# Performance work log

Hardware: AMD Instinct MI355X
Metric: run time of the kernel (lower is better)

The kernel has to match this reference:

```python
import jax, jax.numpy as jnp
import numpy as np

NUM_GROUPS = 32
NUM_HEADS = 8
EPS = 1e-5


def setup_inputs() -> dict:
    key = jax.random.key(0)
    ks = jax.random.split(key, 4)
    b, c, h, w = 16, 512, 32, 32
    x = jax.random.normal(ks[0], (b, c, h, w), dtype=jnp.float32)
    norm_w = jnp.ones((c,), dtype=jnp.float32)
    norm_b = jnp.zeros((c,), dtype=jnp.float32)
    qkv_w = jax.random.normal(ks[1], (3 * c, c), dtype=jnp.float32) * (1.0 / np.sqrt(c))
    qkv_b = jnp.zeros((3 * c,), dtype=jnp.float32)
    proj_w = jax.random.normal(ks[2], (c, c), dtype=jnp.float32) * (1.0 / np.sqrt(c))
    proj_b = jnp.zeros((c,), dtype=jnp.float32)
    return {"x": x, "norm_w": norm_w, "norm_b": norm_b,
            "qkv_w": qkv_w, "qkv_b": qkv_b, "proj_w": proj_w, "proj_b": proj_b}


def group_norm(x, weight, bias):
    b, c, h, w = x.shape
    xg = x.reshape(b, NUM_GROUPS, c // NUM_GROUPS, h * w)
    mean = xg.mean(axis=(2, 3), keepdims=True)
    var = xg.var(axis=(2, 3), keepdims=True)
    xn = (xg - mean) * jax.lax.rsqrt(var + EPS)
    xn = xn.reshape(b, c, h, w)
    return xn * weight[None, :, None, None] + bias[None, :, None, None]


def reference(x, norm_w, norm_b, qkv_w, qkv_b, proj_w, proj_b):
    b, c, h, w = x.shape
    n = h * w
    head = NUM_HEADS
    ch = c // head

    x_norm = group_norm(x, norm_w, norm_b)
    # 1x1 conv == channel matmul: [b,3c,n]
    xf = x_norm.reshape(b, c, n)
    qkv = jnp.einsum('oc,bcn->bon', qkv_w, xf) + qkv_b[None, :, None]
    q, k, v = jnp.split(qkv, 3, axis=1)  # each [b,c,n]
    q = q.reshape(b, head, ch, n) * (ch ** -0.5)
    k = k.reshape(b, head, ch, n)
    v = v.reshape(b, head, ch, n)

    attn = jnp.einsum('bhcn,bhcm->bhnm', q, k)
    attn = jax.nn.softmax(attn, axis=-1)
    out = jnp.einsum('bhnm,bhcm->bhcn', attn, v)  # [b,head,ch,n]
    out = out.reshape(b, c, n)
    out = jnp.einsum('oc,bcn->bon', proj_w, out) + proj_b[None, :, None]
    return x + out.reshape(b, c, h, w)
```

## Files before the change

### kernel.cpp

```cpp
#include <hip/hip_runtime.h>

typedef short short8 __attribute__((ext_vector_type(8)));
typedef float f32x4 __attribute__((ext_vector_type(4)));

#define B_   16
#define C_   512
#define N_   1024
#define NH_  8
#define CH_  64
#define G_   32
#define CPG_ 16

__device__ inline float b2f(unsigned int u) {
    union { unsigned int i; float f; } v; v.i = u << 16; return v.f;
}
__device__ inline unsigned short f2b(float f) {
    union { float f; unsigned int i; } v; v.f = f;
    unsigned int r = v.i + 0x7fffu + ((v.i >> 16) & 1u);
    return (unsigned short)(r >> 16);
}
__device__ inline unsigned int pack2(float a, float b) {
    return (unsigned int)f2b(a) | ((unsigned int)f2b(b) << 16);
}
__device__ inline unsigned int asu(float f) {
    union { float f; unsigned int i; } v; v.f = f; return v.i;
}
__device__ inline unsigned int packtr(float a, float b) {
    return __builtin_amdgcn_perm(asu(b), asu(a), 0x07060302u);
}

__global__ __launch_bounds__(256) void conv_w(const float* __restrict__ qkvw,
                                              const float* __restrict__ projw,
                                              unsigned short* __restrict__ wq,
                                              unsigned short* __restrict__ wp)
{
    const int NQ = 3 * C_ * C_;
    int idx = (blockIdx.x * 256 + threadIdx.x) * 8;
    const float* src; unsigned short* dst; int j;
    if (idx < NQ) { src = qkvw; dst = wq; j = idx; }
    else          { src = projw; dst = wp; j = idx - NQ; }
    float4 u0 = *(const float4*)(src + j);
    float4 u1 = *(const float4*)(src + j + 4);
    uint4 p;
    p.x = pack2(u0.x, u0.y); p.y = pack2(u0.z, u0.w);
    p.z = pack2(u1.x, u1.y); p.w = pack2(u1.z, u1.w);
    *(uint4*)(dst + j) = p;
}

__global__ __launch_bounds__(256) void gn_kernel(const float* __restrict__ x,
                                                 const float* __restrict__ nw,
                                                 const float* __restrict__ nb,
                                                 unsigned short* __restrict__ xnT)
{
    int b = blockIdx.x >> 5, g = blockIdx.x & 31;
    int t = threadIdx.x;
    const float* base = x + ((size_t)(b * C_ + g * CPG_)) * N_;

    float s = 0.f, ss = 0.f;
    for (int it = 0; it < 16; ++it) {
        int idx = (it * 256 + t) * 4;
        float4 u = *(const float4*)(base + idx);
        s  += u.x + u.y + u.z + u.w;
        ss += u.x * u.x + u.y * u.y + u.z * u.z + u.w * u.w;
    }
#pragma unroll
    for (int off = 1; off < 64; off <<= 1) {
        s  += __shfl_xor(s, off);
        ss += __shfl_xor(ss, off);
    }
    __shared__ float red[8];
    int wv = t >> 6;
    if ((t & 63) == 0) { red[wv * 2] = s; red[wv * 2 + 1] = ss; }
    __syncthreads();
    s  = red[0] + red[2] + red[4] + red[6];
    ss = red[1] + red[3] + red[5] + red[7];
    float mean = s * (1.f / 16384.f);
    float var  = ss * (1.f / 16384.f) - mean * mean;
    float rstd = rsqrtf(var + 1e-5f);

    int cl = t >> 4, nn4 = (t & 15) * 4;
    float sc = nw[g * CPG_ + cl] * rstd;
    float sh = nb[g * CPG_ + cl] - mean * sc;
    int nlB = t >> 2, c4 = (t & 3) * 4;

    __shared__ unsigned short T[64 * 17];
    for (int ch = 0; ch < 16; ++ch) {
        int n0 = ch * 64;
        float4 u = *(const float4*)(base + (size_t)cl * N_ + n0 + nn4);
        T[(nn4 + 0) * 17 + cl] = f2b(u.x * sc + sh);
        T[(nn4 + 1) * 17 + cl] = f2b(u.y * sc + sh);
        T[(nn4 + 2) * 17 + cl] = f2b(u.z * sc + sh);
        T[(nn4 + 3) * 17 + cl] = f2b(u.w * sc + sh);
        __syncthreads();
        ushort4 o;
        o.x = T[nlB * 17 + c4 + 0];
        o.y = T[nlB * 17 + c4 + 1];
        o.z = T[nlB * 17 + c4 + 2];
        o.w = T[nlB * 17 + c4 + 3];
        *(ushort4*)(xnT + ((size_t)(b * N_ + n0 + nlB)) * C_ + g * CPG_ + c4) = o;
        __syncthreads();
    }
}

__global__ __launch_bounds__(256) void qkv_kernel(const unsigned short* __restrict__ w,
                                                  const float* __restrict__ bias,
                                                  const unsigned short* __restrict__ xnT,
                                                  unsigned short* __restrict__ qT,
                                                  unsigned short* __restrict__ kT,
                                                  unsigned short* __restrict__ vv)
{
    const int LDA = 40;
    __shared__ unsigned short Als[128 * 40], Bls[128 * 40];
    int t = threadIdx.x;
    int n0 = blockIdx.x * 128, m0 = blockIdx.y * 128, b = blockIdx.z;
    int lane = t & 63, wv = t >> 6;
    int l = lane & 15, qd = lane >> 4;
    int wm = (wv >> 1) * 64, wn = (wv & 1) * 64;
    f32x4 acc[4][4] = {};
    const unsigned short* Bbase = xnT + ((size_t)(b * N_ + n0)) * C_;

    for (int kk = 0; kk < 16; ++kk) {
#pragma unroll
        for (int s_ = 0; s_ < 2; ++s_) {
            int idx = s_ * 256 + t;
            int row = idx >> 2, c8 = (idx & 3) * 8;
            *(uint4*)&Als[row * LDA + c8] = *(const uint4*)(w + (size_t)(m0 + row) * C_ + kk * 32 + c8);
            *(uint4*)&Bls[row * LDA + c8] = *(const uint4*)(Bbase + (size_t)row * C_ + kk * 32 + c8);
        }
        __syncthreads();
        short8 aF[4], bF[4];
#pragma unroll
        for (int i = 0; i < 4; ++i) {
            aF[i] = *(const short8*)&Als[(wm + i * 16 + l) * LDA + qd * 8];
            bF[i] = *(const short8*)&Bls[(wn + i * 16 + l) * LDA + qd * 8];
        }
#pragma unroll
        for (int mt = 0; mt < 4; ++mt)
#pragma unroll
            for (int nt = 0; nt < 4; ++nt)
                acc[mt][nt] = __builtin_amdgcn_mfma_f32_16x16x32_bf16(aF[mt], bF[nt], acc[mt][nt], 0, 0, 0);
        __syncthreads();
    }

    int o_base = m0 + wm;
    int sec = o_base >> 9;
    int oc = o_base & 511;
    int h = oc >> 6;
    float bv[4][4];
#pragma unroll
    for (int mt = 0; mt < 4; ++mt)
#pragma unroll
        for (int r = 0; r < 4; ++r)
            bv[mt][r] = bias[o_base + mt * 16 + qd * 4 + r];

    if (sec < 2) {
        unsigned short* dst = (sec == 0) ? qT : kT;
        float scl = (sec == 0) ? (0.125f * 1.44269504f) : 1.0f;
#pragma unroll
        for (int mt = 0; mt < 4; ++mt)
#pragma unroll
            for (int nt = 0; nt < 4; ++nt) {
                int n = n0 + wn + nt * 16 + l;
                ushort4 o;
                o.x = f2b((acc[mt][nt][0] + bv[mt][0]) * scl);
                o.y = f2b((acc[mt][nt][1] + bv[mt][1]) * scl);
                o.z = f2b((acc[mt][nt][2] + bv[mt][2]) * scl);
                o.w = f2b((acc[mt][nt][3] + bv[mt][3]) * scl);
                *(ushort4*)(dst + ((size_t)(b * NH_ + h) * N_ + n) * CH_ + mt * 16 + qd * 4) = o;
            }
    } else {
#pragma unroll
        for (int mt = 0; mt < 4; ++mt)
#pragma unroll
            for (int nt = 0; nt < 4; ++nt) {
                int n = n0 + wn + nt * 16 + l;
#pragma unroll
                for (int r = 0; r < 4; ++r) {
                    int ch = mt * 16 + qd * 4 + r;
                    vv[((size_t)(b * NH_ + h) * CH_ + ch) * N_ + n] = f2b(acc[mt][nt][r] + bv[mt][r]);
                }
            }
    }
}

__global__ __launch_bounds__(256, 4) void attn_kernel(const unsigned short* __restrict__ qT,
                                                      const unsigned short* __restrict__ kT,
                                                      const unsigned short* __restrict__ vv,
                                                      unsigned short* __restrict__ at)
{
    __shared__ unsigned short Ks[2][4096];
    __shared__ unsigned short Vs[2][4096];

    int t = threadIdx.x, lane = t & 63, wv = t >> 6;
    int l = lane & 15, qd = lane >> 4;
    int blk = blockIdx.x;
    int ibk = blk >> 7;
    int bh  = blk & 127;
    int h = bh & 7, b = bh >> 3;
    int i0 = ibk * 128 + wv * 32;
    const size_t hoff = (size_t)bh * (size_t)N_ * CH_;
    const unsigned short* qbase = qT + hoff;
    const unsigned short* kbase = kT + hoff;
    const unsigned short* vbase = vv + hoff;

    short8 qF[2][2];
#pragma unroll
    for (int it = 0; it < 2; ++it)
#pragma unroll
        for (int ks = 0; ks < 2; ++ks)
            qF[it][ks] = *(const short8*)(qbase + (size_t)(i0 + it * 16 + l) * CH_ + ks * 32 + qd * 8);

    int srow = t >> 2, sc16 = (t & 3) * 16;
    int sw = srow & 7, bb = (t & 3) * 2;
    int d0 = srow * 64 + ((bb ^ sw) * 8);
    int d1 = srow * 64 + (((bb + 1) ^ sw) * 8);
    const unsigned short* kSrc = kbase + (size_t)srow * CH_ + sc16;
    const unsigned short* vSrc = vbase + (size_t)srow * N_ + sc16;

    f32x4 Oa[4][2] = {};
    float lsum[2] = {0.f, 0.f};
    int la0 = (qd & 1) * 32 + l;
    int la1 = la0 + 16;
    int swl = l & 7;

    uint4 ku0, ku1, vu0, vu1;
    {
        const uint4* kp = (const uint4*)(kSrc);
        ku0 = kp[0]; ku1 = kp[1];
        const uint4* vp2 = (const uint4*)(vSrc);
        vu0 = vp2[0]; vu1 = vp2[1];
        *(uint4*)&Ks[0][d0] = ku0; *(uint4*)&Ks[0][d1] = ku1;
        *(uint4*)&Vs[0][d0] = vu0; *(uint4*)&Vs[0][d1] = vu1;
        kp  = (const uint4*)(kSrc + 4096);
        ku0 = kp[0]; ku1 = kp[1];
        vp2 = (const uint4*)(vSrc + 64);
        vu0 = vp2[0]; vu1 = vp2[1];
    }

    for (int tile = 0; tile < 16; ++tile) {
        __syncthreads();
        if (tile < 15) {
            unsigned short* Kw = Ks[(tile + 1) & 1];
            unsigned short* Vw = Vs[(tile + 1) & 1];
            *(uint4*)&Kw[d0] = ku0; *(uint4*)&Kw[d1] = ku1;
            *(uint4*)&Vw[d0] = vu0; *(uint4*)&Vw[d1] = vu1;
            if (tile < 14) {
                const uint4* kp = (const uint4*)(kSrc + (size_t)(tile + 2) * 4096);
                ku0 = kp[0]; ku1 = kp[1];
                const uint4* vp2 = (const uint4*)(vSrc + (size_t)(tile + 2) * 64);
                vu0 = vp2[0]; vu1 = vp2[1];
            }
        }
        const unsigned short* Kb = Ks[tile & 1];
        const unsigned short* Vb = Vs[tile & 1];
#pragma unroll
        for (int jb = 0; jb < 2; ++jb) {
            short8 kA[2][2];
#pragma unroll
            for (int jt = 0; jt < 2; ++jt)
#pragma unroll
                for (int ks = 0; ks < 2; ++ks)
                    kA[jt][ks] = *(const short8*)&Kb[(jb * 32 + jt * 16 + l) * 64 + (((ks * 4 + qd) ^ swl) * 8)];
            f32x4 Sa[2][2] = {};
#pragma unroll
            for (int jt = 0; jt < 2; ++jt)
#pragma unroll
                for (int it = 0; it < 2; ++it)
#pragma unroll
                    for (int ks = 0; ks < 2; ++ks)
                        Sa[jt][it] = __builtin_amdgcn_mfma_f32_16x16x32_bf16(kA[jt][ks], qF[it][ks], Sa[jt][it], 0, 0, 0);
            unsigned int pk[2][2][2];
#pragma unroll
            for (int jt = 0; jt < 2; ++jt)
#pragma unroll
                for (int it = 0; it < 2; ++it) {
                    float p0 = __builtin_amdgcn_exp2f(Sa[jt][it][0]);
                    float p1 = __builtin_amdgcn_exp2f(Sa[jt][it][1]);
                    float p2 = __builtin_amdgcn_exp2f(Sa[jt][it][2]);
                    float p3 = __builtin_amdgcn_exp2f(Sa[jt][it][3]);
                    lsum[it] += (p0 + p1) + (p2 + p3);
                    pk[jt][it][0] = packtr(p0, p1);
                    pk[jt][it][1] = packtr(p2, p3);
                }
            short8 bP[2];
#pragma unroll
            for (int it = 0; it < 2; ++it) {
                union { short8 s; unsigned int u[4]; } fb;
                unsigned int a0 = (unsigned int)__shfl((int)pk[0][it][0], la0);
                unsigned int b0 = (unsigned int)__shfl((int)pk[1][it][0], la0);
                fb.u[0] = (qd < 2) ? a0 : b0;
                unsigned int a1 = (unsigned int)__shfl((int)pk[0][it][1], la0);
                unsigned int b1 = (unsigned int)__shfl((int)pk[1][it][1], la0);
                fb.u[1] = (qd < 2) ? a1 : b1;
                unsigned int a2 = (unsigned int)__shfl((int)pk[0][it][0], la1);
                unsigned int b2 = (unsigned int)__shfl((int)pk[1][it][0], la1);
                fb.u[2] = (qd < 2) ? a2 : b2;
                unsigned int a3 = (unsigned int)__shfl((int)pk[0][it][1], la1);
                unsigned int b3 = (unsigned int)__shfl((int)pk[1][it][1], la1);
                fb.u[3] = (qd < 2) ? a3 : b3;
                bP[it] = fb.s;
            }
            short8 vA[4];
#pragma unroll
            for (int cht = 0; cht < 4; ++cht)
                vA[cht] = *(const short8*)&Vb[(cht * 16 + l) * 64 + (((jb * 4 + qd) ^ swl) * 8)];
#pragma unroll
            for (int cht = 0; cht < 4; ++cht)
#pragma unroll
                for (int it = 0; it < 2; ++it)
                    Oa[cht][it] = __builtin_amdgcn_mfma_f32_16x16x32_bf16(vA[cht], bP[it], Oa[cht][it], 0, 0, 0);
        }
    }

#pragma unroll
    for (int it = 0; it < 2; ++it) {
        float lt = lsum[it];
        lt += __shfl_xor(lt, 16);
        lt += __shfl_xor(lt, 32);
        float inv = 1.0f / lt;
        int i = i0 + it * 16 + l;
        unsigned short* dst = at + ((size_t)(b * N_ + i)) * C_ + h * CH_;
#pragma unroll
        for (int cht = 0; cht < 4; ++cht) {
            ushort4 o;
            o.x = f2b(Oa[cht][it][0] * inv);
            o.y = f2b(Oa[cht][it][1] * inv);
            o.z = f2b(Oa[cht][it][2] * inv);
            o.w = f2b(Oa[cht][it][3] * inv);
            *(ushort4*)(dst + cht * 16 + qd * 4) = o;
        }
    }
}

__global__ __launch_bounds__(256) void proj_kernel(const unsigned short* __restrict__ w,
                                                   const float* __restrict__ bias,
                                                   const unsigned short* __restrict__ at,
                                                   const float* __restrict__ x,
                                                   float* __restrict__ out)
{
    const int LDA = 40;
    __shared__ unsigned short Als[128 * 40], Bls[128 * 40];
    int t = threadIdx.x;
    int n0 = blockIdx.x * 128, m0 = blockIdx.y * 128, b = blockIdx.z;
    int lane = t & 63, wv = t >> 6;
    int l = lane & 15, qd = lane >> 4;
    int wm = (wv >> 1) * 64, wn = (wv & 1) * 64;
    f32x4 acc[4][4] = {};
    const unsigned short* Bbase = at + ((size_t)(b * N_ + n0)) * C_;

    for (int kk = 0; kk < 16; ++kk) {
#pragma unroll
        for (int s_ = 0; s_ < 2; ++s_) {
            int idx = s_ * 256 + t;
            int row = idx >> 2, c8 = (idx & 3) * 8;
            *(uint4*)&Als[row * LDA + c8] = *(const uint4*)(w + (size_t)(m0 + row) * C_ + kk * 32 + c8);
            *(uint4*)&Bls[row * LDA + c8] = *(const uint4*)(Bbase + (size_t)row * C_ + kk * 32 + c8);
        }
        __syncthreads();
        short8 aF[4], bF[4];
#pragma unroll
        for (int i = 0; i < 4; ++i) {
            aF[i] = *(const short8*)&Als[(wm + i * 16 + l) * LDA + qd * 8];
            bF[i] = *(const short8*)&Bls[(wn + i * 16 + l) * LDA + qd * 8];
        }
#pragma unroll
        for (int mt = 0; mt < 4; ++mt)
#pragma unroll
            for (int nt = 0; nt < 4; ++nt)
                acc[mt][nt] = __builtin_amdgcn_mfma_f32_16x16x32_bf16(aF[mt], bF[nt], acc[mt][nt], 0, 0, 0);
        __syncthreads();
    }

    float bv[4][4];
#pragma unroll
    for (int mt = 0; mt < 4; ++mt)
#pragma unroll
        for (int r = 0; r < 4; ++r)
            bv[mt][r] = bias[m0 + wm + mt * 16 + qd * 4 + r];

#pragma unroll
    for (int mt = 0; mt < 4; ++mt)
#pragma unroll
        for (int nt = 0; nt < 4; ++nt) {
            int n = n0 + wn + nt * 16 + l;
#pragma unroll
            for (int r = 0; r < 4; ++r) {
                int o = m0 + wm + mt * 16 + qd * 4 + r;
                size_t idx = ((size_t)b * C_ + o) * N_ + n;
                out[idx] = acc[mt][nt][r] + bv[mt][r] + x[idx];
            }
        }
}

extern "C" void kernel_launch(void* const* d_in, const int* in_sizes, int n_in,
                              void* d_out, int out_size, void* d_ws, size_t ws_size,
                              hipStream_t stream) {
    const float* x     = (const float*)d_in[0];
    const float* nw    = (const float*)d_in[1];
    const float* nb    = (const float*)d_in[2];
    const float* qkvw  = (const float*)d_in[3];
    const float* qkvb  = (const float*)d_in[4];
    const float* projw = (const float*)d_in[5];
    const float* projb = (const float*)d_in[6];
    float* out = (float*)d_out;
    char* ws = (char*)d_ws;
    const size_t SZ = (size_t)B_ * N_ * C_ * 2;
    unsigned short* xnT = (unsigned short*)(ws);
    unsigned short* qTp = (unsigned short*)(ws + SZ);
    unsigned short* kTp = (unsigned short*)(ws + 2 * SZ);
    unsigned short* vp  = (unsigned short*)(ws + 3 * SZ);
    unsigned short* atp = (unsigned short*)(ws);
    unsigned short* wq  = (unsigned short*)(ws + 4 * SZ);
    unsigned short* wp  = (unsigned short*)(ws + 4 * SZ + (size_t)3 * C_ * C_ * 2);

    hipLaunchKernelGGL(conv_w,      dim3(512), dim3(256), 0, stream, qkvw, projw, wq, wp);
    hipLaunchKernelGGL(gn_kernel,   dim3(B_ * G_), dim3(256), 0, stream, x, nw, nb, xnT);
    hipLaunchKernelGGL(qkv_kernel,  dim3(8, 12, B_), dim3(256), 0, stream, wq, qkvb, xnT, qTp, kTp, vp);
    hipLaunchKernelGGL(attn_kernel, dim3(1024), dim3(256), 0, stream, qTp, kTp, vp, atp);
    hipLaunchKernelGGL(proj_kernel, dim3(8, 4, B_), dim3(256), 0, stream, wp, projb, atp, x, out);
}
```

Measured before the change: 227.3 us.

## Merge GN and weight conversion, use direct-to-LDS loads and permlane swaps

Merges the weight bf16 conversion and group norm into one launch, which saves a kernel launch. The qkv and proj GEMMs now stage tiles with global_load_lds into XOR-swizzled, unpadded LDS instead of going through registers with a padded layout. In attention, the P-fragment transpose uses v_permlane32/16_swap instead of many __shfl calls, guarded by a runtime check that falls back to shuffles. The GEMM loop still waits on all loads with no double buffering, so load latency stays exposed.

```diff
diff --git a/kernel.cpp b/kernel.cpp
--- a/kernel.cpp
+++ b/kernel.cpp
@@ -28,32 +28,41 @@
 __device__ inline unsigned int packtr(float a, float b) {
     return __builtin_amdgcn_perm(asu(b), asu(a), 0x07060302u);
 }
-
-__global__ __launch_bounds__(256) void conv_w(const float* __restrict__ qkvw,
-                                              const float* __restrict__ projw,
-                                              unsigned short* __restrict__ wq,
-                                              unsigned short* __restrict__ wp)
+__device__ inline void gload16(const void* g, void* l) {
+    __builtin_amdgcn_global_load_lds(
+        (const __attribute__((address_space(1))) void*)g,
+        (__attribute__((address_space(3))) void*)l, 16, 0, 0);
+}
+
+__global__ __launch_bounds__(256) void gnconv_kernel(const float* __restrict__ x,
+                                                     const float* __restrict__ nw,
+                                                     const float* __restrict__ nb,
+                                                     unsigned short* __restrict__ xnT,
+                                                     const float* __restrict__ qkvw,
+                                                     const float* __restrict__ projw,
+                                                     unsigned short* __restrict__ wq,
+                                                     unsigned short* __restrict__ wp)
 {
-    const int NQ = 3 * C_ * C_;
-    int idx = (blockIdx.x * 256 + threadIdx.x) * 8;
-    const float* src; unsigned short* dst; int j;
-    if (idx < NQ) { src = qkvw; dst = wq; j = idx; }
-    else          { src = projw; dst = wp; j = idx - NQ; }
-    float4 u0 = *(const float4*)(src + j);
-    float4 u1 = *(const float4*)(src + j + 4);
-    uint4 p;
-    p.x = pack2(u0.x, u0.y); p.y = pack2(u0.z, u0.w);
-    p.z = pack2(u1.x, u1.y); p.w = pack2(u1.z, u1.w);
-    *(uint4*)(dst + j) = p;
-}
-
-__global__ __launch_bounds__(256) void gn_kernel(const float* __restrict__ x,
-                                                 const float* __restrict__ nw,
-                                                 const float* __restrict__ nb,
-                                                 unsigned short* __restrict__ xnT)
-{
+    __shared__ float red[8];
+    __shared__ unsigned short T[64 * 17];
+    int t = threadIdx.x;
+
+    if (blockIdx.x >= 512) {
+        const int NQ = 3 * C_ * C_;
+        int idx = (((int)blockIdx.x - 512) * 256 + t) * 8;
+        const float* src; unsigned short* dst; int j;
+        if (idx < NQ) { src = qkvw;  dst = wq; j = idx; }
+        else          { src = projw; dst = wp; j = idx - NQ; }
+        float4 u0 = *(const float4*)(src + j);
+        float4 u1 = *(const float4*)(src + j + 4);
+        uint4 p;
+        p.x = pack2(u0.x, u0.y); p.y = pack2(u0.z, u0.w);
+        p.z = pack2(u1.x, u1.y); p.w = pack2(u1.z, u1.w);
+        *(uint4*)(dst + j) = p;
+        return;
+    }
+
     int b = blockIdx.x >> 5, g = blockIdx.x & 31;
-    int t = threadIdx.x;
     const float* base = x + ((size_t)(b * C_ + g * CPG_)) * N_;
 
     float s = 0.f, ss = 0.f;
@@ -68,7 +77,6 @@
         s  += __shfl_xor(s, off);
         ss += __shfl_xor(ss, off);
     }
-    __shared__ float red[8];
     int wv = t >> 6;
     if ((t & 63) == 0) { red[wv * 2] = s; red[wv * 2 + 1] = ss; }
     __syncthreads();
@@ -83,7 +91,6 @@
     float sh = nb[g * CPG_ + cl] - mean * sc;
     int nlB = t >> 2, c4 = (t & 3) * 4;
 
-    __shared__ unsigned short T[64 * 17];
     for (int ch = 0; ch < 16; ++ch) {
         int n0 = ch * 64;
         float4 u = *(const float4*)(base + (size_t)cl * N_ + n0 + nn4);
@@ -109,8 +116,7 @@
                                                   unsigned short* __restrict__ kT,
                                                   unsigned short* __restrict__ vv)
 {
-    const int LDA = 40;
-    __shared__ unsigned short Als[128 * 40], Bls[128 * 40];
+    __shared__ unsigned short Als[128 * 32], Bls[128 * 32];
     int t = threadIdx.x;
     int n0 = blockIdx.x * 128, m0 = blockIdx.y * 128, b = blockIdx.z;
     int lane = t & 63, wv = t >> 6;
@@ -119,20 +125,39 @@
     f32x4 acc[4][4] = {};
     const unsigned short* Bbase = xnT + ((size_t)(b * N_ + n0)) * C_;
 
+    int lr = lane >> 2, bpos = lane & 3;
+    int r0 = wv * 32 + lr, r1 = r0 + 16;
+    int c0 = (bpos ^ ((r0 >> 1) & 3)) * 8;
+    int c1 = (bpos ^ ((r1 >> 1) & 3)) * 8;
+    const unsigned short* gA0 = w + (size_t)(m0 + r0) * C_ + c0;
+    const unsigned short* gA1 = w + (size_t)(m0 + r1) * C_ + c1;
+    const unsigned short* gB0 = Bbase + (size_t)r0 * C_ + c0;
+    const unsigned short* gB1 = Bbase + (size_t)r1 * C_ + c1;
+    unsigned short* lA0 = &Als[(wv * 32) * 32];
+    unsigned short* lA1 = &Als[(wv * 32 + 16) * 32];
+    unsigned short* lB0 = &Bls[(wv * 32) * 32];
+    unsigned short* lB1 = &Bls[(wv * 32 + 16) * 32];
+
+    int aoff[4], boff[4];
+#pragma unroll
+    for (int i = 0; i < 4; ++i) {
+        int ra = wm + i * 16 + l;
+        aoff[i] = ra * 32 + ((qd ^ ((ra >> 1) & 3)) * 8);
+        int rb = wn + i * 16 + l;
+        boff[i] = rb * 32 + ((qd ^ ((rb >> 1) & 3)) * 8);
+    }
+
     for (int kk = 0; kk < 16; ++kk) {
-#pragma unroll
-        for (int s_ = 0; s_ < 2; ++s_) {
-            int idx = s_ * 256 + t;
-            int row = idx >> 2, c8 = (idx & 3) * 8;
-            *(uint4*)&Als[row * LDA + c8] = *(const uint4*)(w + (size_t)(m0 + row) * C_ + kk * 32 + c8);
-            *(uint4*)&Bls[row * LDA + c8] = *(const uint4*)(Bbase + (size_t)row * C_ + kk * 32 + c8);
-        }
+        int ko = kk * 32;
+        gload16(gA0 + ko, lA0); gload16(gA1 + ko, lA1);
+        gload16(gB0 + ko, lB0); gload16(gB1 + ko, lB1);
+        __builtin_amdgcn_s_waitcnt(0);
         __syncthreads();
         short8 aF[4], bF[4];
 #pragma unroll
         for (int i = 0; i < 4; ++i) {
-            aF[i] = *(const short8*)&Als[(wm + i * 16 + l) * LDA + qd * 8];
-            bF[i] = *(const short8*)&Bls[(wn + i * 16 + l) * LDA + qd * 8];
+            aF[i] = *(const short8*)&Als[aoff[i]];
+            bF[i] = *(const short8*)&Bls[boff[i]];
         }
 #pragma unroll
         for (int mt = 0; mt < 4; ++mt)
@@ -202,6 +227,15 @@
     const unsigned short* qbase = qT + hoff;
     const unsigned short* kbase = kT + hoff;
     const unsigned short* vbase = vv + hoff;
+
+    int plok;
+    {
+        unsigned int ta = (unsigned int)lane, tb = 64u + (unsigned int)lane;
+        asm volatile("v_permlane32_swap_b32 %0, %1" : "+v"(ta), "+v"(tb));
+        asm volatile("v_permlane16_swap_b32 %0, %1" : "+v"(ta), "+v"(tb));
+        unsigned int e1 = (unsigned int)((lane >> 4) * 32 + (lane & 15));
+        plok = __all(ta == e1) && __all(tb == e1 + 16u);
+    }
 
     short8 qF[2][2];
 #pragma unroll
@@ -283,22 +317,37 @@
                     pk[jt][it][1] = packtr(p2, p3);
                 }
             short8 bP[2];
-#pragma unroll
-            for (int it = 0; it < 2; ++it) {
-                union { short8 s; unsigned int u[4]; } fb;
-                unsigned int a0 = (unsigned int)__shfl((int)pk[0][it][0], la0);
-                unsigned int b0 = (unsigned int)__shfl((int)pk[1][it][0], la0);
-                fb.u[0] = (qd < 2) ? a0 : b0;
-                unsigned int a1 = (unsigned int)__shfl((int)pk[0][it][1], la0);
-                unsigned int b1 = (unsigned int)__shfl((int)pk[1][it][1], la0);
-                fb.u[1] = (qd < 2) ? a1 : b1;
-                unsigned int a2 = (unsigned int)__shfl((int)pk[0][it][0], la1);
-                unsigned int b2 = (unsigned int)__shfl((int)pk[1][it][0], la1);
-                fb.u[2] = (qd < 2) ? a2 : b2;
-                unsigned int a3 = (unsigned int)__shfl((int)pk[0][it][1], la1);
-                unsigned int b3 = (unsigned int)__shfl((int)pk[1][it][1], la1);
-                fb.u[3] = (qd < 2) ? a3 : b3;
-                bP[it] = fb.s;
+            if (plok) {
+#pragma unroll
+                for (int it = 0; it < 2; ++it) {
+                    union { short8 s; unsigned int u[4]; } fb;
+                    unsigned int a0 = pk[0][it][0], c0 = pk[1][it][0];
+                    asm volatile("v_permlane32_swap_b32 %0, %1" : "+v"(a0), "+v"(c0));
+                    asm volatile("v_permlane16_swap_b32 %0, %1" : "+v"(a0), "+v"(c0));
+                    unsigned int a1 = pk[0][it][1], c1 = pk[1][it][1];
+                    asm volatile("v_permlane32_swap_b32 %0, %1" : "+v"(a1), "+v"(c1));
+                    asm volatile("v_permlane16_swap_b32 %0, %1" : "+v"(a1), "+v"(c1));
+                    fb.u[0] = a0; fb.u[1] = a1; fb.u[2] = c0; fb.u[3] = c1;
+                    bP[it] = fb.s;
+                }
+            } else {
+#pragma unroll
+                for (int it = 0; it < 2; ++it) {
+                    union { short8 s; unsigned int u[4]; } fb;
+                    unsigned int a0 = (unsigned int)__shfl((int)pk[0][it][0], la0);
+                    unsigned int b0 = (unsigned int)__shfl((int)pk[1][it][0], la0);
+                    fb.u[0] = (qd < 2) ? a0 : b0;
+                    unsigned int a1 = (unsigned int)__shfl((int)pk[0][it][1], la0);
+                    unsigned int b1 = (unsigned int)__shfl((int)pk[1][it][1], la0);
+                    fb.u[1] = (qd < 2) ? a1 : b1;
+                    unsigned int a2 = (unsigned int)__shfl((int)pk[0][it][0], la1);
+                    unsigned int b2 = (unsigned int)__shfl((int)pk[1][it][0], la1);
+                    fb.u[2] = (qd < 2) ? a2 : b2;
+                    unsigned int a3 = (unsigned int)__shfl((int)pk[0][it][1], la1);
+                    unsigned int b3 = (unsigned int)__shfl((int)pk[1][it][1], la1);
+                    fb.u[3] = (qd < 2) ? a3 : b3;
+                    bP[it] = fb.s;
+                }
             }
             short8 vA[4];
 #pragma unroll
@@ -338,8 +387,7 @@
                                                    const float* __restrict__ x,
                                                    float* __restrict__ out)
 {
-    const int LDA = 40;
-    __shared__ unsigned short Als[128 * 40], Bls[128 * 40];
+    __shared__ unsigned short Als[128 * 32], Bls[128 * 32];
     int t = threadIdx.x;
     int n0 = blockIdx.x * 128, m0 = blockIdx.y * 128, b = blockIdx.z;
     int lane = t & 63, wv = t >> 6;
@@ -348,20 +396,39 @@
     f32x4 acc[4][4] = {};
     const unsigned short* Bbase = at + ((size_t)(b * N_ + n0)) * C_;
 
+    int lr = lane >> 2, bpos = lane & 3;
+    int r0 = wv * 32 + lr, r1 = r0 + 16;
+    int c0 = (bpos ^ ((r0 >> 1) & 3)) * 8;
+    int c1 = (bpos ^ ((r1 >> 1) & 3)) * 8;
+    const unsigned short* gA0 = w + (size_t)(m0 + r0) * C_ + c0;
+    const unsigned short* gA1 = w + (size_t)(m0 + r1) * C_ + c1;
+    const unsigned short* gB0 = Bbase + (size_t)r0 * C_ + c0;
+    const unsigned short* gB1 = Bbase + (size_t)r1 * C_ + c1;
+    unsigned short* lA0 = &Als[(wv * 32) * 32];
+    unsigned short* lA1 = &Als[(wv * 32 + 16) * 32];
+    unsigned short* lB0 = &Bls[(wv * 32) * 32];
+    unsigned short* lB1 = &Bls[(wv * 32 + 16) * 32];
+
+    int aoff[4], boff[4];
+#pragma unroll
+    for (int i = 0; i < 4; ++i) {
+        int ra = wm + i * 16 + l;
+        aoff[i] = ra * 32 + ((qd ^ ((ra >> 1) & 3)) * 8);
+        int rb = wn + i * 16 + l;
+        boff[i] = rb * 32 + ((qd ^ ((rb >> 1) & 3)) * 8);
+    }
+
     for (int kk = 0; kk < 16; ++kk) {
-#pragma unroll
-        for (int s_ = 0; s_ < 2; ++s_) {
-            int idx = s_ * 256 + t;
-            int row = idx >> 2, c8 = (idx & 3) * 8;
-            *(uint4*)&Als[row * LDA + c8] = *(const uint4*)(w + (size_t)(m0 + row) * C_ + kk * 32 + c8);
-            *(uint4*)&Bls[row * LDA + c8] = *(const uint4*)(Bbase + (size_t)row * C_ + kk * 32 + c8);
-        }
+        int ko = kk * 32;
+        gload16(gA0 + ko, lA0); gload16(gA1 + ko, lA1);
+        gload16(gB0 + ko, lB0); gload16(gB1 + ko, lB1);
+        __builtin_amdgcn_s_waitcnt(0);
         __syncthreads();
         short8 aF[4], bF[4];
 #pragma unroll
         for (int i = 0; i < 4; ++i) {
-            aF[i] = *(const short8*)&Als[(wm + i * 16 + l) * LDA + qd * 8];
-            bF[i] = *(const short8*)&Bls[(wn + i * 16 + l) * LDA + qd * 8];
+            aF[i] = *(const short8*)&Als[aoff[i]];
+            bF[i] = *(const short8*)&Bls[boff[i]];
         }
 #pragma unroll
         for (int mt = 0; mt < 4; ++mt)
@@ -413,9 +480,8 @@
     unsigned short* wq  = (unsigned short*)(ws + 4 * SZ);
     unsigned short* wp  = (unsigned short*)(ws + 4 * SZ + (size_t)3 * C_ * C_ * 2);
 
-    hipLaunchKernelGGL(conv_w,      dim3(512), dim3(256), 0, stream, qkvw, projw, wq, wp);
-    hipLaunchKernelGGL(gn_kernel,   dim3(B_ * G_), dim3(256), 0, stream, x, nw, nb, xnT);
-    hipLaunchKernelGGL(qkv_kernel,  dim3(8, 12, B_), dim3(256), 0, stream, wq, qkvb, xnT, qTp, kTp, vp);
-    hipLaunchKernelGGL(attn_kernel, dim3(1024), dim3(256), 0, stream, qTp, kTp, vp, atp);
-    hipLaunchKernelGGL(proj_kernel, dim3(8, 4, B_), dim3(256), 0, stream, wp, projb, atp, x, out);
-}
+    hipLaunchKernelGGL(gnconv_kernel, dim3(1024), dim3(256), 0, stream, x, nw, nb, xnT, qkvw, projw, wq, wp);
+    hipLaunchKernelGGL(qkv_kernel,    dim3(8, 12, B_), dim3(256), 0, stream, wq, qkvb, xnT, qTp, kTp, vp);
+    hipLaunchKernelGGL(attn_kernel,   dim3(1024), dim3(256), 0, stream, qTp, kTp, vp, atp);
+    hipLaunchKernelGGL(proj_kernel,   dim3(8, 4, B_), dim3(256), 0, stream, wp, projb, atp, x, out);
+}
```

Result: faster. 219.1 us (-3.6%).
